# Kernel tuning notes

Hardware: AMD Instinct MI355X
Metric: run time of the kernel (lower is better)

## Reference

```python
import jax, jax.numpy as jnp
import numpy as np

NUM_CAPSULE = 32
DIM_CAPSULE = 32
ROUTINGS = 3
T_EPSILON = 1e-7


def setup_inputs() -> dict:
    key = jax.random.key(0)
    k1, k2 = jax.random.split(key)
    x = jax.random.normal(k1, (64, 1024, 256), dtype=jnp.float32)
    # xavier_normal_ on [1, 256, 32*32]: std = sqrt(2/(fan_in+fan_out)) = sqrt(2/(256+1024))
    std = np.sqrt(2.0 / (256 + NUM_CAPSULE * DIM_CAPSULE)).astype(np.float32)
    W = jax.random.normal(k2, (1, 256, NUM_CAPSULE * DIM_CAPSULE), dtype=jnp.float32) * std
    return {"x": x, "W": W}


def _squash(v, eps):
    # x / sqrt(sum(x^2) + eps)  (note: not the classic squash; faithful to source)
    s = jnp.sum(v * v, axis=-1, keepdims=True)
    return v / jnp.sqrt(s + eps)


def reference(x, W):
    B, N_in, _ = x.shape
    # u_hat: [B, num_capsule, input_num_capsule, dim_capsule]
    u_hat = jnp.matmul(x, W).reshape(B, N_in, NUM_CAPSULE, DIM_CAPSULE)
    u_hat = jnp.transpose(u_hat, (0, 2, 1, 3))
    b = jnp.zeros(u_hat.shape[:3], dtype=u_hat.dtype)  # [B, num, n_in]
    outputs = None
    for i in range(ROUTINGS):
        # original: softmax over the num_capsule axis (dim=2 after permute(0,2,1))
        c = jax.nn.softmax(b, axis=1)  # [B, num, n_in]
        outputs = _squash(jnp.einsum('bij,bijk->bik', c, u_hat), T_EPSILON)  # [B, num, dim]
        if i < ROUTINGS - 1:
            b = jnp.einsum('bik,bijk->bij', outputs, u_hat)
    return outputs
```

## Files before the change

kernel.cpp:

```cpp
#include <hip/hip_runtime.h>
#include <cstdint>
#include <cstddef>

#define BATCH 64
#define NIN   1024
#define CIN   256
#define NC    32
#define NJC   16
#define JCH   64
#define T_EPS 1e-7f
#define CT_S  72

typedef __attribute__((ext_vector_type(8))) short short8;
typedef __attribute__((ext_vector_type(4))) float floatx4;

__device__ __forceinline__ unsigned short bf16rne(float f) {
  unsigned int u = __float_as_uint(f);
  u += 0x7FFFu + ((u >> 16) & 1u);
  return (unsigned short)(u >> 16);
}
__device__ __forceinline__ float bf2f(unsigned short h) {
  return __uint_as_float(((unsigned int)h) << 16);
}
__device__ __forceinline__ int xsw(int j, int c) {
  return j * 256 + ((((c >> 3) ^ (j & 7) ^ ((j >> 3) & 7)) << 3) | (c & 7));
}

union USH {
  unsigned short cT[NC * CT_S];
};

__global__ __launch_bounds__(256) void k_colsum(const float* __restrict__ x,
                                                const float* __restrict__ W,
                                                unsigned short* __restrict__ Wi,
                                                unsigned short* __restrict__ WiT,
                                                float* __restrict__ y0p) {
  const int jc = blockIdx.x, b = blockIdx.y, t = threadIdx.x;
  const int jj = t >> 6, c4 = t & 63;
  __shared__ float4 red[4][64];
  const float4* xg = (const float4*)(x + ((size_t)(b * NIN + jc * JCH)) * CIN);
  float4 acc = make_float4(0.f, 0.f, 0.f, 0.f);
  #pragma unroll
  for (int jr = 0; jr < 16; ++jr) {
    int j = jr * 4 + jj;
    float4 v = xg[j * 64 + c4];
    acc.x += v.x; acc.y += v.y; acc.z += v.z; acc.w += v.w;
  }
  red[jj][c4] = acc;
  if (b == 0) {
    #pragma unroll
    for (int i2 = 0; i2 < 2; ++i2) {
      int i = jc * 2 + i2;
      const float4* wsrc = (const float4*)(W + (size_t)t * 1024 + i * 32);
      unsigned short* wdst = Wi + ((size_t)i * CIN + t) * NC;
      unsigned short* wtd  = WiT + (size_t)i * 32 * CIN + t;
      #pragma unroll
      for (int k4 = 0; k4 < 8; ++k4) {
        float4 v = wsrc[k4];
        ushort4 h;
        h.x = bf16rne(v.x); h.y = bf16rne(v.y);
        h.z = bf16rne(v.z); h.w = bf16rne(v.w);
        *(ushort4*)&wdst[k4 * 4] = h;
        wtd[(size_t)(k4 * 4 + 0) * CIN] = h.x;
        wtd[(size_t)(k4 * 4 + 1) * CIN] = h.y;
        wtd[(size_t)(k4 * 4 + 2) * CIN] = h.z;
        wtd[(size_t)(k4 * 4 + 3) * CIN] = h.w;
      }
    }
  }
  __syncthreads();
  if (t < 64) {
    float4 s = red[0][t];
    #pragma unroll
    for (int p = 1; p < 4; ++p) {
      s.x += red[p][t].x; s.y += red[p][t].y;
      s.z += red[p][t].z; s.w += red[p][t].w;
    }
    *(float4*)&y0p[(b * NJC + jc) * CIN + t * 4] = s;
  }
}

template <int MODE>
__global__ __launch_bounds__(256) void k_post(const void* __restrict__ yin,
                                              const unsigned short* __restrict__ Wi,
                                              const unsigned short* __restrict__ WiT,
                                              unsigned short* __restrict__ wtout,
                                              float* __restrict__ outg) {
  const int i = blockIdx.x, b = blockIdx.y, t = threadIdx.x;
  const int k = t & 31, g = t >> 5;
  __shared__ float ys[CIN];
  __shared__ float sred[8][32];
  __shared__ float os[NC];
  short8 wv[4];
  {
    const short8* wtrow = (const short8*)(WiT + ((size_t)i * 32 + k) * CIN + g * 32);
    #pragma unroll
    for (int m = 0; m < 4; ++m) wv[m] = wtrow[m];
  }
  short8 wr[4];
  if constexpr (MODE != 2) {
    const short8* wrow = (const short8*)(Wi + ((size_t)i * CIN + t) * NC);
    #pragma unroll
    for (int m = 0; m < 4; ++m) wr[m] = wrow[m];
  }
  float a = 0.f;
  if (MODE == 0) {
    const float* y0p = (const float*)yin;
    #pragma unroll
    for (int p = 0; p < NJC; ++p) a += y0p[(b * NJC + p) * CIN + t];
    a *= (1.f / 32.f);
  } else {
    const unsigned short* yp = (const unsigned short*)yin;
    #pragma unroll
    for (int p = 0; p < NJC; ++p)
      a += bf2f(yp[(((size_t)(b * NJC + p)) * NC + i) * CIN + t]);
  }
  ys[t] = a;
  __syncthreads();
  {
    float ps = 0.f;
    #pragma unroll
    for (int m = 0; m < 4; ++m)
      #pragma unroll
      for (int e = 0; e < 8; ++e)
        ps += ys[g * 32 + m * 8 + e] * bf2f((unsigned short)wv[m][e]);
    sred[g][k] = ps;
  }
  __syncthreads();
  float s = 0.f;
  #pragma unroll
  for (int g8 = 0; g8 < 8; ++g8) s += sred[g8][k];
  float s2 = s * s;
  #pragma unroll
  for (int m = 1; m < 32; m <<= 1) s2 += __shfl_xor(s2, m);
  float o = s * rsqrtf(s2 + T_EPS);
  if constexpr (MODE == 2) {
    if (t < 32) outg[((size_t)b * NC + i) * 32 + t] = o;
  } else {
    if (t < 32) os[t] = o;
    __syncthreads();
    float acc = 0.f;
    #pragma unroll
    for (int k8 = 0; k8 < 4; ++k8) {
      #pragma unroll
      for (int e = 0; e < 8; ++e)
        acc += os[k8 * 8 + e] * bf2f((unsigned short)wr[k8][e]);
    }
    wtout[((size_t)b * NC + i) * CIN + t] = bf16rne(acc);
  }
}

__device__ __forceinline__ void fused_iter(int b, int t,
                                           const unsigned short* xs, USH* u,
                                           const unsigned short* __restrict__ wt,
                                           short8 a0p0, short8 a1p0,
                                           short8 a0p1, short8 a1p1,
                                           unsigned short* __restrict__ yo) {
  const int w = t >> 6, l16 = t & 15, q = (t >> 4) & 3;
  const int jloc = w * 16 + l16;
  const unsigned short* wrow = wt + (size_t)b * NC * CIN;
  floatx4 accA0 = {0.f, 0.f, 0.f, 0.f}, accA1 = {0.f, 0.f, 0.f, 0.f};
  {
    short8 bx0 = *(const short8*)&xs[xsw(jloc, 0 * 32 + q * 8)];
    accA0 = __builtin_amdgcn_mfma_f32_16x16x32_bf16(a0p0, bx0, accA0, 0, 0, 0);
    accA1 = __builtin_amdgcn_mfma_f32_16x16x32_bf16(a1p0, bx0, accA1, 0, 0, 0);
    short8 bx1 = *(const short8*)&xs[xsw(jloc, 1 * 32 + q * 8)];
    accA0 = __builtin_amdgcn_mfma_f32_16x16x32_bf16(a0p1, bx1, accA0, 0, 0, 0);
    accA1 = __builtin_amdgcn_mfma_f32_16x16x32_bf16(a1p1, bx1, accA1, 0, 0, 0);
  }
  #pragma unroll
  for (int ks = 2; ks < 8; ++ks) {
    short8 bx = *(const short8*)&xs[xsw(jloc, ks * 32 + q * 8)];
    short8 a0 = *(const short8*)(wrow + (size_t)l16 * CIN + ks * 32 + q * 8);
    short8 a1 = *(const short8*)(wrow + (size_t)(16 + l16) * CIN + ks * 32 + q * 8);
    accA0 = __builtin_amdgcn_mfma_f32_16x16x32_bf16(a0, bx, accA0, 0, 0, 0);
    accA1 = __builtin_amdgcn_mfma_f32_16x16x32_bf16(a1, bx, accA1, 0, 0, 0);
  }
  {
    float m = accA0[0];
    #pragma unroll
    for (int r = 1; r < 4; ++r) m = fmaxf(m, accA0[r]);
    #pragma unroll
    for (int r = 0; r < 4; ++r) m = fmaxf(m, accA1[r]);
    m = fmaxf(m, __shfl_xor(m, 16));
    m = fmaxf(m, __shfl_xor(m, 32));
    float e0[4], e1[4], s = 0.f;
    #pragma unroll
    for (int r = 0; r < 4; ++r) {
      e0[r] = __expf(accA0[r] - m);
      e1[r] = __expf(accA1[r] - m);
      s += e0[r] + e1[r];
    }
    s += __shfl_xor(s, 16);
    s += __shfl_xor(s, 32);
    float rs = 1.f / s;
    #pragma unroll
    for (int r = 0; r < 4; ++r) {
      u->cT[(q * 4 + r) * CT_S + jloc]      = bf16rne(e0[r] * rs);
      u->cT[(16 + q * 4 + r) * CT_S + jloc] = bf16rne(e1[r] * rs);
    }
  }
  __syncthreads();
  const int cw = w * 64;
  floatx4 accB[2][4];
  #pragma unroll
  for (int h = 0; h < 2; ++h)
    #pragma unroll
    for (int ct = 0; ct < 4; ++ct) accB[h][ct] = (floatx4){0.f, 0.f, 0.f, 0.f};
  #pragma unroll
  for (int ks = 0; ks < 2; ++ks) {
    short8 ca0 = *(const short8*)&u->cT[l16 * CT_S + ks * 32 + q * 8];
    short8 ca1 = *(const short8*)&u->cT[(16 + l16) * CT_S + ks * 32 + q * 8];
    #pragma unroll
    for (int ct = 0; ct < 4; ++ct) {
      const int c = cw + ct * 16 + l16;
      short8 xf;
      #pragma unroll
      for (int e = 0; e < 8; ++e)
        xf[e] = (short)xs[xsw(ks * 32 + q * 8 + e, c)];
      accB[0][ct] = __builtin_amdgcn_mfma_f32_16x16x32_bf16(ca0, xf, accB[0][ct], 0, 0, 0);
      accB[1][ct] = __builtin_amdgcn_mfma_f32_16x16x32_bf16(ca1, xf, accB[1][ct], 0, 0, 0);
    }
  }
  #pragma unroll
  for (int h = 0; h < 2; ++h)
    #pragma unroll
    for (int ct = 0; ct < 4; ++ct)
      #pragma unroll
      for (int r = 0; r < 4; ++r) {
        int i = h * 16 + q * 4 + r;
        int c = cw + ct * 16 + l16;
        yo[i * CIN + c] = bf16rne(accB[h][ct][r]);
      }
}

__global__ __launch_bounds__(256, 4) void k_fusedf(const float* __restrict__ x,
                                                   const unsigned short* __restrict__ wt,
                                                   unsigned short* __restrict__ ypart) {
  const int jc = blockIdx.x, b = blockIdx.y, t = threadIdx.x;
  const int l16 = t & 15, q = (t >> 4) & 3;
  __shared__ unsigned short xs[64 * 256];
  __shared__ USH u;
  const unsigned short* wrow = wt + (size_t)b * NC * CIN;
  short8 a0p0 = *(const short8*)(wrow + (size_t)l16 * CIN + 0 * 32 + q * 8);
  short8 a1p0 = *(const short8*)(wrow + (size_t)(16 + l16) * CIN + 0 * 32 + q * 8);
  short8 a0p1 = *(const short8*)(wrow + (size_t)l16 * CIN + 1 * 32 + q * 8);
  short8 a1p1 = *(const short8*)(wrow + (size_t)(16 + l16) * CIN + 1 * 32 + q * 8);
  {
    const int jj = t >> 6, c4 = t & 63;
    const float4* xg = (const float4*)(x + ((size_t)(b * NIN + jc * JCH)) * CIN);
    #pragma unroll
    for (int jr = 0; jr < 16; ++jr) {
      int j = jr * 4 + jj;
      float4 v = xg[j * 64 + c4];
      ushort4 h;
      h.x = bf16rne(v.x); h.y = bf16rne(v.y);
      h.z = bf16rne(v.z); h.w = bf16rne(v.w);
      *(ushort4*)&xs[xsw(j, c4 * 4)] = h;
    }
  }
  __syncthreads();
  fused_iter(b, t, xs, &u, wt, a0p0, a1p0, a0p1, a1p1,
             ypart + ((size_t)(b * NJC + jc)) * NC * CIN);
}


extern "C" void kernel_launch(void* const* d_in, const int* in_sizes, int n_in,
                              void* d_out, int out_size, void* d_ws, size_t ws_size,
                              hipStream_t stream) {
  (void)in_sizes; (void)n_in; (void)out_size; (void)ws_size;
  const float* x = (const float*)d_in[0];
  const float* W = (const float*)d_in[1];
  float* out = (float*)d_out;
  char* ws = (char*)d_ws;
  unsigned short* wtb   = (unsigned short*)ws;
  unsigned short* ypart = (unsigned short*)(ws + (1ull << 20));
  float*          y0p   = (float*)(ws + (17ull << 20));
  unsigned short* Wi    = (unsigned short*)(ws + (18ull << 20));
  unsigned short* WiT   = (unsigned short*)(ws + (18ull << 20) + (512ull << 10));

  dim3 gfuse(NJC, BATCH);
  dim3 gpost(NC, BATCH);
  k_colsum<<<gfuse, 256, 0, stream>>>(x, W, Wi, WiT, y0p);
  k_post<0><<<gpost, 256, 0, stream>>>(y0p, Wi, WiT, wtb, nullptr);
  k_fusedf<<<gfuse, 256, 0, stream>>>(x, wtb, ypart);
  k_post<1><<<gpost, 256, 0, stream>>>(ypart, Wi, WiT, wtb, nullptr);
  k_fusedf<<<gfuse, 256, 0, stream>>>(x, wtb, ypart);
  k_post<2><<<gpost, 256, 0, stream>>>(ypart, Wi, WiT, nullptr, out);
}
```

Baseline: 158.9 us.

## Load x fragments directly into registers and store transposed swizzled tile in LDS

The fused routing kernel now has each thread load its own x row fragment from global memory straight into registers, converting it to bf16 and feeding the first MFMA stage without staging through LDS. The same values are written to a transposed, XOR-swizzled LDS tile (channel-major), so the second MFMA stage can read a contiguous short8 per lane instead of gathering eight scalar shorts. This removes the barrier between the x load and the first GEMM and cuts the LDS reads in the second GEMM. In exchange it issues scalar LDS stores for the transpose, holds more registers per thread, and uses global loads that are less coalesced, since each thread reads its own row.

```diff
diff --git a/kernel.cpp b/kernel.cpp
--- a/kernel.cpp
+++ b/kernel.cpp
@@ -22,8 +22,8 @@
 __device__ __forceinline__ float bf2f(unsigned short h) {
   return __uint_as_float(((unsigned int)h) << 16);
 }
-__device__ __forceinline__ int xsw(int j, int c) {
-  return j * 256 + ((((c >> 3) ^ (j & 7) ^ ((j >> 3) & 7)) << 3) | (c & 7));
+__device__ __forceinline__ int xtsw(int c, int j) {
+  return c * 64 + (j ^ ((((c) ^ ((c) >> 3)) & 7) << 3));
 }
 
 union USH {
@@ -150,118 +150,107 @@
   }
 }
 
-__device__ __forceinline__ void fused_iter(int b, int t,
-                                           const unsigned short* xs, USH* u,
-                                           const unsigned short* __restrict__ wt,
-                                           short8 a0p0, short8 a1p0,
-                                           short8 a0p1, short8 a1p1,
-                                           unsigned short* __restrict__ yo) {
-  const int w = t >> 6, l16 = t & 15, q = (t >> 4) & 3;
-  const int jloc = w * 16 + l16;
-  const unsigned short* wrow = wt + (size_t)b * NC * CIN;
-  floatx4 accA0 = {0.f, 0.f, 0.f, 0.f}, accA1 = {0.f, 0.f, 0.f, 0.f};
-  {
-    short8 bx0 = *(const short8*)&xs[xsw(jloc, 0 * 32 + q * 8)];
-    accA0 = __builtin_amdgcn_mfma_f32_16x16x32_bf16(a0p0, bx0, accA0, 0, 0, 0);
-    accA1 = __builtin_amdgcn_mfma_f32_16x16x32_bf16(a1p0, bx0, accA1, 0, 0, 0);
-    short8 bx1 = *(const short8*)&xs[xsw(jloc, 1 * 32 + q * 8)];
-    accA0 = __builtin_amdgcn_mfma_f32_16x16x32_bf16(a0p1, bx1, accA0, 0, 0, 0);
-    accA1 = __builtin_amdgcn_mfma_f32_16x16x32_bf16(a1p1, bx1, accA1, 0, 0, 0);
-  }
-  #pragma unroll
-  for (int ks = 2; ks < 8; ++ks) {
-    short8 bx = *(const short8*)&xs[xsw(jloc, ks * 32 + q * 8)];
-    short8 a0 = *(const short8*)(wrow + (size_t)l16 * CIN + ks * 32 + q * 8);
-    short8 a1 = *(const short8*)(wrow + (size_t)(16 + l16) * CIN + ks * 32 + q * 8);
-    accA0 = __builtin_amdgcn_mfma_f32_16x16x32_bf16(a0, bx, accA0, 0, 0, 0);
-    accA1 = __builtin_amdgcn_mfma_f32_16x16x32_bf16(a1, bx, accA1, 0, 0, 0);
-  }
-  {
-    float m = accA0[0];
-    #pragma unroll
-    for (int r = 1; r < 4; ++r) m = fmaxf(m, accA0[r]);
-    #pragma unroll
-    for (int r = 0; r < 4; ++r) m = fmaxf(m, accA1[r]);
-    m = fmaxf(m, __shfl_xor(m, 16));
-    m = fmaxf(m, __shfl_xor(m, 32));
-    float e0[4], e1[4], s = 0.f;
-    #pragma unroll
-    for (int r = 0; r < 4; ++r) {
-      e0[r] = __expf(accA0[r] - m);
-      e1[r] = __expf(accA1[r] - m);
-      s += e0[r] + e1[r];
-    }
-    s += __shfl_xor(s, 16);
-    s += __shfl_xor(s, 32);
-    float rs = 1.f / s;
-    #pragma unroll
-    for (int r = 0; r < 4; ++r) {
-      u->cT[(q * 4 + r) * CT_S + jloc]      = bf16rne(e0[r] * rs);
-      u->cT[(16 + q * 4 + r) * CT_S + jloc] = bf16rne(e1[r] * rs);
-    }
-  }
-  __syncthreads();
-  const int cw = w * 64;
-  floatx4 accB[2][4];
-  #pragma unroll
-  for (int h = 0; h < 2; ++h)
-    #pragma unroll
-    for (int ct = 0; ct < 4; ++ct) accB[h][ct] = (floatx4){0.f, 0.f, 0.f, 0.f};
-  #pragma unroll
-  for (int ks = 0; ks < 2; ++ks) {
-    short8 ca0 = *(const short8*)&u->cT[l16 * CT_S + ks * 32 + q * 8];
-    short8 ca1 = *(const short8*)&u->cT[(16 + l16) * CT_S + ks * 32 + q * 8];
-    #pragma unroll
-    for (int ct = 0; ct < 4; ++ct) {
-      const int c = cw + ct * 16 + l16;
-      short8 xf;
-      #pragma unroll
-      for (int e = 0; e < 8; ++e)
-        xf[e] = (short)xs[xsw(ks * 32 + q * 8 + e, c)];
-      accB[0][ct] = __builtin_amdgcn_mfma_f32_16x16x32_bf16(ca0, xf, accB[0][ct], 0, 0, 0);
-      accB[1][ct] = __builtin_amdgcn_mfma_f32_16x16x32_bf16(ca1, xf, accB[1][ct], 0, 0, 0);
-    }
-  }
-  #pragma unroll
-  for (int h = 0; h < 2; ++h)
-    #pragma unroll
-    for (int ct = 0; ct < 4; ++ct)
-      #pragma unroll
-      for (int r = 0; r < 4; ++r) {
-        int i = h * 16 + q * 4 + r;
-        int c = cw + ct * 16 + l16;
-        yo[i * CIN + c] = bf16rne(accB[h][ct][r]);
-      }
-}
-
-__global__ __launch_bounds__(256, 4) void k_fusedf(const float* __restrict__ x,
+__global__ __launch_bounds__(256, 4) void k_fusedr(const float* __restrict__ x,
                                                    const unsigned short* __restrict__ wt,
                                                    unsigned short* __restrict__ ypart) {
   const int jc = blockIdx.x, b = blockIdx.y, t = threadIdx.x;
-  const int l16 = t & 15, q = (t >> 4) & 3;
-  __shared__ unsigned short xs[64 * 256];
+  const int w = t >> 6, l16 = t & 15, q = (t >> 4) & 3;
+  const int jloc = w * 16 + l16;
+  __shared__ __align__(16) unsigned short xT[CIN * JCH];
   __shared__ USH u;
   const unsigned short* wrow = wt + (size_t)b * NC * CIN;
   short8 a0p0 = *(const short8*)(wrow + (size_t)l16 * CIN + 0 * 32 + q * 8);
   short8 a1p0 = *(const short8*)(wrow + (size_t)(16 + l16) * CIN + 0 * 32 + q * 8);
   short8 a0p1 = *(const short8*)(wrow + (size_t)l16 * CIN + 1 * 32 + q * 8);
   short8 a1p1 = *(const short8*)(wrow + (size_t)(16 + l16) * CIN + 1 * 32 + q * 8);
+  const float4* xg = (const float4*)(x + ((size_t)(b * NIN + jc * JCH) + jloc) * CIN);
+  float4 xv[16];
+  #pragma unroll
+  for (int ks = 0; ks < 8; ++ks) {
+    xv[ks * 2]     = xg[ks * 8 + q * 2];
+    xv[ks * 2 + 1] = xg[ks * 8 + q * 2 + 1];
+  }
+  short8 bxf[8];
+  #pragma unroll
+  for (int ks = 0; ks < 8; ++ks) {
+    float f[8] = {xv[ks * 2].x,     xv[ks * 2].y,     xv[ks * 2].z,     xv[ks * 2].w,
+                  xv[ks * 2 + 1].x, xv[ks * 2 + 1].y, xv[ks * 2 + 1].z, xv[ks * 2 + 1].w};
+    short8 h8;
+    #pragma unroll
+    for (int e = 0; e < 8; ++e) h8[e] = (short)bf16rne(f[e]);
+    bxf[ks] = h8;
+    #pragma unroll
+    for (int e = 0; e < 8; ++e) {
+      int c = ks * 32 + q * 8 + e;
+      xT[xtsw(c, jloc)] = (unsigned short)h8[e];
+    }
+  }
+  floatx4 accA0 = {0.f, 0.f, 0.f, 0.f}, accA1 = {0.f, 0.f, 0.f, 0.f};
+  accA0 = __builtin_amdgcn_mfma_f32_16x16x32_bf16(a0p0, bxf[0], accA0, 0, 0, 0);
+  accA1 = __builtin_amdgcn_mfma_f32_16x16x32_bf16(a1p0, bxf[0], accA1, 0, 0, 0);
+  accA0 = __builtin_amdgcn_mfma_f32_16x16x32_bf16(a0p1, bxf[1], accA0, 0, 0, 0);
+  accA1 = __builtin_amdgcn_mfma_f32_16x16x32_bf16(a1p1, bxf[1], accA1, 0, 0, 0);
+  #pragma unroll
+  for (int ks = 2; ks < 8; ++ks) {
+    short8 a0 = *(const short8*)(wrow + (size_t)l16 * CIN + ks * 32 + q * 8);
+    short8 a1 = *(const short8*)(wrow + (size_t)(16 + l16) * CIN + ks * 32 + q * 8);
+    accA0 = __builtin_amdgcn_mfma_f32_16x16x32_bf16(a0, bxf[ks], accA0, 0, 0, 0);
+    accA1 = __builtin_amdgcn_mfma_f32_16x16x32_bf16(a1, bxf[ks], accA1, 0, 0, 0);
+  }
   {
-    const int jj = t >> 6, c4 = t & 63;
-    const float4* xg = (const float4*)(x + ((size_t)(b * NIN + jc * JCH)) * CIN);
-    #pragma unroll
-    for (int jr = 0; jr < 16; ++jr) {
-      int j = jr * 4 + jj;
-      float4 v = xg[j * 64 + c4];
-      ushort4 h;
-      h.x = bf16rne(v.x); h.y = bf16rne(v.y);
-      h.z = bf16rne(v.z); h.w = bf16rne(v.w);
-      *(ushort4*)&xs[xsw(j, c4 * 4)] = h;
-    }
-  }
-  __syncthreads();
-  fused_iter(b, t, xs, &u, wt, a0p0, a1p0, a0p1, a1p1,
-             ypart + ((size_t)(b * NJC + jc)) * NC * CIN);
+    float m = accA0[0];
+    #pragma unroll
+    for (int r = 1; r < 4; ++r) m = fmaxf(m, accA0[r]);
+    #pragma unroll
+    for (int r = 0; r < 4; ++r) m = fmaxf(m, accA1[r]);
+    m = fmaxf(m, __shfl_xor(m, 16));
+    m = fmaxf(m, __shfl_xor(m, 32));
+    float e0[4], e1[4], s = 0.f;
+    #pragma unroll
+    for (int r = 0; r < 4; ++r) {
+      e0[r] = __expf(accA0[r] - m);
+      e1[r] = __expf(accA1[r] - m);
+      s += e0[r] + e1[r];
+    }
+    s += __shfl_xor(s, 16);
+    s += __shfl_xor(s, 32);
+    float rs = 1.f / s;
+    #pragma unroll
+    for (int r = 0; r < 4; ++r) {
+      u.cT[(q * 4 + r) * CT_S + jloc]      = bf16rne(e0[r] * rs);
+      u.cT[(16 + q * 4 + r) * CT_S + jloc] = bf16rne(e1[r] * rs);
+    }
+  }
+  __syncthreads();
+  const int cw = w * 64;
+  floatx4 accB[2][4];
+  #pragma unroll
+  for (int h = 0; h < 2; ++h)
+    #pragma unroll
+    for (int ct = 0; ct < 4; ++ct) accB[h][ct] = (floatx4){0.f, 0.f, 0.f, 0.f};
+  #pragma unroll
+  for (int ks = 0; ks < 2; ++ks) {
+    short8 ca0 = *(const short8*)&u.cT[l16 * CT_S + ks * 32 + q * 8];
+    short8 ca1 = *(const short8*)&u.cT[(16 + l16) * CT_S + ks * 32 + q * 8];
+    #pragma unroll
+    for (int ct = 0; ct < 4; ++ct) {
+      const int c = cw + ct * 16 + l16;
+      short8 xf = *(const short8*)&xT[xtsw(c, ks * 32 + q * 8)];
+      accB[0][ct] = __builtin_amdgcn_mfma_f32_16x16x32_bf16(ca0, xf, accB[0][ct], 0, 0, 0);
+      accB[1][ct] = __builtin_amdgcn_mfma_f32_16x16x32_bf16(ca1, xf, accB[1][ct], 0, 0, 0);
+    }
+  }
+  unsigned short* yo = ypart + ((size_t)(b * NJC + jc)) * NC * CIN;
+  #pragma unroll
+  for (int h = 0; h < 2; ++h)
+    #pragma unroll
+    for (int ct = 0; ct < 4; ++ct)
+      #pragma unroll
+      for (int r = 0; r < 4; ++r) {
+        int i = h * 16 + q * 4 + r;
+        int c = cw + ct * 16 + l16;
+        yo[i * CIN + c] = bf16rne(accB[h][ct][r]);
+      }
 }
 
 
@@ -283,8 +272,8 @@
   dim3 gpost(NC, BATCH);
   k_colsum<<<gfuse, 256, 0, stream>>>(x, W, Wi, WiT, y0p);
   k_post<0><<<gpost, 256, 0, stream>>>(y0p, Wi, WiT, wtb, nullptr);
-  k_fusedf<<<gfuse, 256, 0, stream>>>(x, wtb, ypart);
+  k_fusedr<<<gfuse, 256, 0, stream>>>(x, wtb, ypart);
   k_post<1><<<gpost, 256, 0, stream>>>(ypart, Wi, WiT, wtb, nullptr);
-  k_fusedf<<<gfuse, 256, 0, stream>>>(x, wtb, ypart);
+  k_fusedr<<<gfuse, 256, 0, stream>>>(x, wtb, ypart);
   k_post<2><<<gpost, 256, 0, stream>>>(ypart, Wi, WiT, nullptr, out);
 }
```

After: 163.9 us. 1.03x slower.
